# Optimization experiments

Measured on AMD Instinct MI355X. Metric: run time of the kernel, lower is better.

The kernel has to match this reference:

```python
import jax, jax.numpy as jnp
import numpy as np

N_NODES = 100000
N_EDGES = 800000
D_IN = 128
HOPS = 2
BN_EPS = 1e-5


def setup_inputs() -> dict:
    key = jax.random.key(0)
    ks = jax.random.split(key, 12)
    d_cat = D_IN * (HOPS + 1)  # 384
    inp = {
        "x": jax.random.normal(ks[0], (N_NODES, D_IN), dtype=jnp.float32),
        "edge_index": jax.random.randint(ks[1], (2, N_EDGES), 0, N_NODES, dtype=jnp.int32),
        "W0": jax.random.normal(ks[2], (HOPS + 1, D_IN, D_IN), dtype=jnp.float32) / np.sqrt(D_IN),
        "b0": jax.random.normal(ks[3], (HOPS + 1, D_IN), dtype=jnp.float32) * 0.01,
        "W1": jax.random.normal(ks[4], (HOPS + 1, d_cat, D_IN), dtype=jnp.float32) / np.sqrt(d_cat),
        "b1": jax.random.normal(ks[5], (HOPS + 1, D_IN), dtype=jnp.float32) * 0.01,
        "W2": jax.random.normal(ks[6], (HOPS + 1, d_cat, D_IN), dtype=jnp.float32) / np.sqrt(d_cat),
        "b2": jax.random.normal(ks[7], (HOPS + 1, D_IN), dtype=jnp.float32) * 0.01,
        "bn_gamma": jnp.ones((2, d_cat), dtype=jnp.float32),
        "bn_beta": jnp.zeros((2, d_cat), dtype=jnp.float32),
    }
    return inp


def _gcn_norm(edge_index, n):
    # gcn_norm(add_self_loops=False): deg over col, w_e = d^-1/2[row]*d^-1/2[col]
    row, col = edge_index[0], edge_index[1]
    deg = jax.ops.segment_sum(jnp.ones(row.shape[0], jnp.float32), col, num_segments=n)
    dinv = jnp.where(deg > 0, jax.lax.rsqrt(jnp.maximum(deg, 1.0)), 0.0)
    w = dinv[row] * dinv[col]
    return row, col, w


def _spmm(row, col, w, xj, n):
    # adj_t = SparseTensor(row=col, col=row, value=w): out[col_e] += w_e * x[row_e]
    return jax.ops.segment_sum(w[:, None] * xj[row], col, num_segments=n)


def _mixhop_layer(x, W, b, row, col, w, n):
    outs = [x @ W[0] + b[0]]
    for j in range(1, HOPS + 1):
        xj = x @ W[j] + b[j]
        for _ in range(j):
            xj = _spmm(row, col, w, xj, n)
        outs.append(xj)
    return jnp.concatenate(outs, axis=1)


def _bn(x, g, b):
    mu = jnp.mean(x, axis=0)
    var = jnp.mean(jnp.square(x - mu), axis=0)
    return (x - mu) * jax.lax.rsqrt(var + BN_EPS) * g + b


def reference(x, edge_index, W0, b0, W1, b1, W2, b2, bn_gamma, bn_beta):
    n = x.shape[0]
    row, col, w = _gcn_norm(edge_index, n)
    h = _mixhop_layer(x, W0, b0, row, col, w, n)
    h = jax.nn.relu(_bn(h, bn_gamma[0], bn_beta[0]))  # dropout: eval mode (identity)
    h = _mixhop_layer(h, W1, b1, row, col, w, n)
    h = jax.nn.relu(_bn(h, bn_gamma[1], bn_beta[1]))
    h = _mixhop_layer(h, W2, b2, row, col, w, n)
    return h
```

## Files before the change

kernel.cpp:

```cpp
#include <hip/hip_runtime.h>
#include <hip/hip_bf16.h>

#define NN 100000
#define NE 800000
#define DIN 128
#define DCAT 384
#define BN_EPS 1e-5

typedef __attribute__((ext_vector_type(8))) short bf16x8;
typedef __attribute__((ext_vector_type(4))) float f32x4;


__global__ void count_deg_k(const int* __restrict__ ei, int* __restrict__ deg) {
    int i = blockIdx.x * blockDim.x + threadIdx.x;
    if (i < NE) atomicAdd(&deg[ei[NE + i]], 1);
}

__global__ void dinv_k(const int* __restrict__ deg, float* __restrict__ dinv) {
    int i = blockIdx.x * blockDim.x + threadIdx.x;
    if (i < NN) {
        int d = deg[i];
        dinv[i] = (d > 0) ? rsqrtf((float)d) : 0.f;
    }
}

__global__ void scan1_k(const int* __restrict__ deg, int* __restrict__ out,
                        int* __restrict__ bsum) {
    __shared__ int s[1024];
    int i = blockIdx.x * 1024 + threadIdx.x;
    int v = (i < NN) ? deg[i] : 0;
    s[threadIdx.x] = v;
    __syncthreads();
    for (int off = 1; off < 1024; off <<= 1) {
        int t = (threadIdx.x >= off) ? s[threadIdx.x - off] : 0;
        __syncthreads();
        s[threadIdx.x] += t;
        __syncthreads();
    }
    if (i < NN) out[i] = s[threadIdx.x] - v;
    if (threadIdx.x == 1023) bsum[blockIdx.x] = s[1023];
}

__global__ void scan2_k(int* __restrict__ bsum, int nb) {
    if (threadIdx.x == 0) {
        int acc = 0;
        for (int b = 0; b < nb; ++b) { int v = bsum[b]; bsum[b] = acc; acc += v; }
    }
}

__global__ void scan3_k(int* __restrict__ ptr, int* __restrict__ cursor,
                        const int* __restrict__ bsum) {
    int i = blockIdx.x * 1024 + threadIdx.x;
    if (i < NN) {
        int p = ptr[i] + bsum[blockIdx.x];
        ptr[i] = p;
        cursor[i] = p;
    }
    if (i == NN) ptr[NN] = NE;
}

__global__ void scatter_k(const int* __restrict__ ei, const float* __restrict__ dinv,
                          int* __restrict__ cursor, int* __restrict__ crow,
                          float* __restrict__ cw) {
    int i = blockIdx.x * blockDim.x + threadIdx.x;
    if (i >= NE) return;
    int r = ei[i];
    int c = ei[NE + i];
    int p = atomicAdd(&cursor[c], 1);
    crow[p] = r;
    cw[p] = dinv[r] * dinv[c];
}


__device__ inline void split_trunc(float x, short& hi, short& lo) {
    unsigned u = __builtin_bit_cast(unsigned, x);
    hi = (short)(u >> 16);
    float hf = __builtin_bit_cast(float, u & 0xFFFF0000u);
    __hip_bfloat16 l = __float2bfloat16(x - hf);
    lo = *reinterpret_cast<short*>(&l);
}

__global__ void wsplit_k(const float* __restrict__ W, int K,
                         short* __restrict__ Wth, short* __restrict__ Wtl) {
    int i = blockIdx.x * 256 + threadIdx.x;
    if (i >= 3 * K * 128) return;
    int c = i & 127;
    int k = (i >> 7) % K;
    int j = i / (K * 128);
    short h, l;
    split_trunc(W[i], h, l);
    size_t o = (size_t)j * 128 * 384 + (size_t)c * 384 + k;
    Wth[o] = h;
    Wtl[o] = l;
}

#define GPITCH 40

__global__ __launch_bounds__(256, 2) void gemm3m_k(
    const float* __restrict__ X, int K,
    const short* __restrict__ Wth, const short* __restrict__ Wtl,
    const float* __restrict__ bias,
    float* __restrict__ o0, float* __restrict__ o1, float* __restrict__ o2) {
    __shared__ short As_h[128 * GPITCH];
    __shared__ short As_l[128 * GPITCH];
    __shared__ short Bs_h[128 * GPITCH];
    __shared__ short Bs_l[128 * GPITCH];

    const int j    = blockIdx.x;
    const int m0   = blockIdx.y * 128;
    const int t    = threadIdx.x;
    const int lane = t & 63;
    const int wv   = t >> 6;
    const int wr   = (wv >> 1) * 64;
    const int wc   = (wv & 1) * 64;
    const int lr   = lane & 15;
    const int lk   = lane >> 4;

    const short* Wh = Wth + (size_t)j * 128 * 384;
    const short* Wl = Wtl + (size_t)j * 128 * 384;

    f32x4 acc[4][4];
#pragma unroll
    for (int a = 0; a < 4; ++a)
#pragma unroll
        for (int b = 0; b < 4; ++b) acc[a][b] = (f32x4){0.f, 0.f, 0.f, 0.f};

    for (int kb = 0; kb < K; kb += 32) {
#pragma unroll
        for (int i = 0; i < 4; ++i) {
            int lin = t + i * 256;
            int row = lin >> 3, kq = lin & 7;
            int gr = m0 + row;
            if (gr >= NN) gr = NN - 1;
            float4 a4 = *(const float4*)(X + (size_t)gr * K + kb + kq * 4);
            short h0, l0, h1, l1, h2, l2, h3, l3;
            split_trunc(a4.x, h0, l0);
            split_trunc(a4.y, h1, l1);
            split_trunc(a4.z, h2, l2);
            split_trunc(a4.w, h3, l3);
            *(short4*)&As_h[row * GPITCH + kq * 4] = make_short4(h0, h1, h2, h3);
            *(short4*)&As_l[row * GPITCH + kq * 4] = make_short4(l0, l1, l2, l3);
        }
#pragma unroll
        for (int i = 0; i < 4; ++i) {
            int lin = t + i * 256;
            int col = lin >> 3, kq = lin & 7;
            short4 bh = *(const short4*)(Wh + (size_t)col * 384 + kb + kq * 4);
            short4 bl = *(const short4*)(Wl + (size_t)col * 384 + kb + kq * 4);
            *(short4*)&Bs_h[col * GPITCH + kq * 4] = bh;
            *(short4*)&Bs_l[col * GPITCH + kq * 4] = bl;
        }
        __syncthreads();

        bf16x8 ah[4], al[4];
#pragma unroll
        for (int mr = 0; mr < 4; ++mr) {
            int r = wr + mr * 16 + lr;
            ah[mr] = *(const bf16x8*)&As_h[r * GPITCH + lk * 8];
            al[mr] = *(const bf16x8*)&As_l[r * GPITCH + lk * 8];
        }
#pragma unroll
        for (int nc = 0; nc < 4; ++nc) {
            int c = wc + nc * 16 + lr;
            bf16x8 bh = *(const bf16x8*)&Bs_h[c * GPITCH + lk * 8];
            bf16x8 bl = *(const bf16x8*)&Bs_l[c * GPITCH + lk * 8];
#pragma unroll
            for (int mr = 0; mr < 4; ++mr) {
                f32x4 a = acc[mr][nc];
                a = __builtin_amdgcn_mfma_f32_16x16x32_bf16(al[mr], bh, a, 0, 0, 0);
                a = __builtin_amdgcn_mfma_f32_16x16x32_bf16(ah[mr], bl, a, 0, 0, 0);
                a = __builtin_amdgcn_mfma_f32_16x16x32_bf16(ah[mr], bh, a, 0, 0, 0);
                acc[mr][nc] = a;
            }
        }
        __syncthreads();
    }

    float* dst;
    int pitch;
    if (j == 0)      { dst = o0; pitch = DCAT; }
    else if (j == 1) { dst = o1; pitch = 128; }
    else             { dst = o2; pitch = 128; }

#pragma unroll
    for (int nc = 0; nc < 4; ++nc) {
        int col = wc + nc * 16 + lr;
        float bv = bias[j * 128 + col];
#pragma unroll
        for (int mr = 0; mr < 4; ++mr) {
            f32x4 a = acc[mr][nc];
#pragma unroll
            for (int r = 0; r < 4; ++r) {
                int row = m0 + wr + mr * 16 + lk * 4 + r;
                if (row < NN) dst[(size_t)row * pitch + col] = a[r] + bv;
            }
        }
    }
}

__global__ __launch_bounds__(256) void spmm_k(
    const int* __restrict__ ptr, const int* __restrict__ rows,
    const float* __restrict__ wv, const float* __restrict__ xin, int pin,
    float* __restrict__ xout, int pout) {
    int wid  = (blockIdx.x * blockDim.x + threadIdx.x) >> 6;
    int lane = threadIdx.x & 63;
    if (wid >= NN) return;
    int e0 = ptr[wid], e1 = ptr[wid + 1];
    float2 acc = make_float2(0.f, 0.f);
    for (int e = e0; e < e1; ++e) {
        int r   = rows[e];
        float w = wv[e];
        float2 v = ((const float2*)(xin + (size_t)r * pin))[lane];
        acc.x += w * v.x;
        acc.y += w * v.y;
    }
    ((float2*)(xout + (size_t)wid * pout))[lane] = acc;
}

#define BN_ROWS 256
#define BN_NBLK ((NN + BN_ROWS - 1) / BN_ROWS)

__global__ void bn_stats1_k(const float* __restrict__ H, float* __restrict__ partial) {
    int c  = threadIdx.x;
    int r0 = blockIdx.x * BN_ROWS;
    int r1 = min(r0 + BN_ROWS, NN);
    float s = 0.f, s2 = 0.f;
    for (int r = r0; r < r1; ++r) {
        float v = H[(size_t)r * DCAT + c];
        s  += v;
        s2 += v * v;
    }
    partial[blockIdx.x * 768 + c]       = s;
    partial[blockIdx.x * 768 + 384 + c] = s2;
}

__global__ void bn_finalize_k(const float* __restrict__ partial,
                              const float* __restrict__ g, const float* __restrict__ b,
                              float2* __restrict__ coef) {
    int c = threadIdx.x;
    double s = 0.0, s2 = 0.0;
    for (int i = 0; i < BN_NBLK; ++i) {
        s  += (double)partial[i * 768 + c];
        s2 += (double)partial[i * 768 + 384 + c];
    }
    double mu  = s / (double)NN;
    double var = s2 / (double)NN - mu * mu;
    double inv = 1.0 / sqrt(var + (double)BN_EPS);
    float scale = (float)((double)g[c] * inv);
    float shift = (float)((double)b[c] - mu * (double)g[c] * inv);
    coef[c] = make_float2(scale, shift);
}

__global__ void bn_apply_k(float* __restrict__ H, const float2* __restrict__ coef) {
    unsigned i = blockIdx.x * blockDim.x + threadIdx.x;
    if (i >= (unsigned)NN * 96u) return;
    float4 v = ((float4*)H)[i];
    int c4 = (int)(i % 96u) * 4;
    float2 s0 = coef[c4 + 0];
    float2 s1 = coef[c4 + 1];
    float2 s2 = coef[c4 + 2];
    float2 s3 = coef[c4 + 3];
    v.x = fmaxf(v.x * s0.x + s0.y, 0.f);
    v.y = fmaxf(v.y * s1.x + s1.y, 0.f);
    v.z = fmaxf(v.z * s2.x + s2.y, 0.f);
    v.w = fmaxf(v.w * s3.x + s3.y, 0.f);
    ((float4*)H)[i] = v;
}


static void run_layer(const float* X, int K, const float* W, const float* bias,
                      float* Hout, float* tmpA, float* tmpB,
                      short* Wth, short* Wtl,
                      const int* ptr, const int* crow, const float* cw,
                      hipStream_t stream) {
    int nw = 3 * K * 128;
    wsplit_k<<<(nw + 255) / 256, 256, 0, stream>>>(W, K, Wth, Wtl);
    dim3 g(3, (NN + 127) / 128);
    gemm3m_k<<<g, 256, 0, stream>>>(X, K, Wth, Wtl, bias, Hout, tmpA, tmpB);
    int sg = (NN * 64 + 255) / 256;
    spmm_k<<<sg, 256, 0, stream>>>(ptr, crow, cw, tmpA, 128, Hout + 128, DCAT);
    spmm_k<<<sg, 256, 0, stream>>>(ptr, crow, cw, tmpB, 128, tmpA, 128);
    spmm_k<<<sg, 256, 0, stream>>>(ptr, crow, cw, tmpA, 128, Hout + 256, DCAT);
}

static void run_bn(float* H, const float* g, const float* b,
                   float* partial, float2* coef, hipStream_t stream) {
    bn_stats1_k<<<BN_NBLK, 384, 0, stream>>>(H, partial);
    bn_finalize_k<<<1, 384, 0, stream>>>(partial, g, b, coef);
    unsigned n4 = (unsigned)NN * 96u;
    bn_apply_k<<<(n4 + 255) / 256, 256, 0, stream>>>(H, coef);
}

extern "C" void kernel_launch(void* const* d_in, const int* in_sizes, int n_in,
                              void* d_out, int out_size, void* d_ws, size_t ws_size,
                              hipStream_t stream) {
    const float* x        = (const float*)d_in[0];
    const int*   ei       = (const int*)d_in[1];
    const float* W0       = (const float*)d_in[2];
    const float* b0       = (const float*)d_in[3];
    const float* W1       = (const float*)d_in[4];
    const float* b1       = (const float*)d_in[5];
    const float* W2       = (const float*)d_in[6];
    const float* b2       = (const float*)d_in[7];
    const float* bn_gamma = (const float*)d_in[8];
    const float* bn_beta  = (const float*)d_in[9];
    float* out = (float*)d_out;

    char* p = (char*)d_ws;
    auto alloc = [&](size_t bytes) -> void* {
        void* r = (void*)p;
        p += (bytes + 511) & ~(size_t)511;
        return r;
    };
    float* Hws     = (float*)alloc((size_t)NN * DCAT * 4);
    float* tmpA    = (float*)alloc((size_t)NN * 128 * 4);
    float* tmpB    = (float*)alloc((size_t)NN * 128 * 4);
    int*   deg     = (int*)alloc((size_t)NN * 4);
    float* dinv    = (float*)alloc((size_t)NN * 4);
    int*   ptr     = (int*)alloc((size_t)(NN + 1) * 4);
    int*   cursor  = (int*)alloc((size_t)NN * 4);
    int*   bsum    = (int*)alloc(1024);
    int*   crow    = (int*)alloc((size_t)NE * 4);
    float* cw      = (float*)alloc((size_t)NE * 4);
    float* partial = (float*)alloc((size_t)BN_NBLK * 768 * 4);
    float2* coef   = (float2*)alloc(384 * 8);
    short* Wth     = (short*)alloc((size_t)3 * 128 * 384 * 2);
    short* Wtl     = (short*)alloc((size_t)3 * 128 * 384 * 2);

    hipMemsetAsync(deg, 0, (size_t)NN * 4, stream);
    count_deg_k<<<(NE + 255) / 256, 256, 0, stream>>>(ei, deg);
    dinv_k<<<(NN + 255) / 256, 256, 0, stream>>>(deg, dinv);
    int nsb = (NN + 1023) / 1024;
    scan1_k<<<nsb, 1024, 0, stream>>>(deg, ptr, bsum);
    scan2_k<<<1, 64, 0, stream>>>(bsum, nsb);
    scan3_k<<<nsb, 1024, 0, stream>>>(ptr, cursor, bsum);
    scatter_k<<<(NE + 255) / 256, 256, 0, stream>>>(ei, dinv, cursor, crow, cw);

    run_layer(x, DIN, W0, b0, out, tmpA, tmpB, Wth, Wtl, ptr, crow, cw, stream);
    run_bn(out, bn_gamma, bn_beta, partial, coef, stream);

    run_layer(out, DCAT, W1, b1, Hws, tmpA, tmpB, Wth, Wtl, ptr, crow, cw, stream);
    run_bn(Hws, bn_gamma + DCAT, bn_beta + DCAT, partial, coef, stream);

    run_layer(Hws, DCAT, W2, b2, out, tmpA, tmpB, Wth, Wtl, ptr, crow, cw, stream);
}
```

Before: 1.918 ms.

## Fuse BN apply into GEMM prologue, merge SpMMs, swizzle GEMM grid, unroll SpMM

Drops the separate batchnorm+ReLU pass by applying scale/shift/ReLU while loading GEMM A tiles, which removes a full read-write of the 100000x384 activation per layer. The first-hop SpMM and the first half of the two-hop SpMM are merged into one kernel that reads each edge list once and gathers both inputs. The GEMM grid is flattened with an XCD-aware swizzle so blocks sharing weights land on the same XCD. The SpMM edge loops are also unrolled for more memory-level parallelism. Risks: the GEMM A-load path gets heavier, and buffers are reused across layers (out/Hws as scratch), which needs careful aliasing.

New measurement: 1.702 ms. 1.13x faster.

```diff
diff --git a/kernel.cpp b/kernel.cpp
--- a/kernel.cpp
+++ b/kernel.cpp
@@ -100,14 +100,22 @@
     const float* __restrict__ X, int K,
     const short* __restrict__ Wth, const short* __restrict__ Wtl,
     const float* __restrict__ bias,
+    const float2* __restrict__ coef, int use_bn,
     float* __restrict__ o0, float* __restrict__ o1, float* __restrict__ o2) {
     __shared__ short As_h[128 * GPITCH];
     __shared__ short As_l[128 * GPITCH];
     __shared__ short Bs_h[128 * GPITCH];
     __shared__ short Bs_l[128 * GPITCH];
 
-    const int j    = blockIdx.x;
-    const int m0   = blockIdx.y * 128;
+    const int nwg = gridDim.x;
+    const int id  = blockIdx.x;
+    const int q = nwg >> 3, r = nwg & 7;
+    const int xcd = id & 7, ii = id >> 3;
+    const int swz = (xcd < r ? xcd * (q + 1) : r * (q + 1) + (xcd - r) * q) + ii;
+    const int j  = swz % 3;
+    const int my = swz / 3;
+    const int m0 = my * 128;
+
     const int t    = threadIdx.x;
     const int lane = t & 63;
     const int wv   = t >> 6;
@@ -133,6 +141,14 @@
             int gr = m0 + row;
             if (gr >= NN) gr = NN - 1;
             float4 a4 = *(const float4*)(X + (size_t)gr * K + kb + kq * 4);
+            if (use_bn) {
+                int c = kb + kq * 4;
+                float2 c0 = coef[c + 0], c1 = coef[c + 1], c2 = coef[c + 2], c3 = coef[c + 3];
+                a4.x = fmaxf(a4.x * c0.x + c0.y, 0.f);
+                a4.y = fmaxf(a4.y * c1.x + c1.y, 0.f);
+                a4.z = fmaxf(a4.z * c2.x + c2.y, 0.f);
+                a4.w = fmaxf(a4.w * c3.x + c3.y, 0.f);
+            }
             short h0, l0, h1, l1, h2, l2, h3, l3;
             split_trunc(a4.x, h0, l0);
             split_trunc(a4.y, h1, l1);
@@ -155,9 +171,9 @@
         bf16x8 ah[4], al[4];
 #pragma unroll
         for (int mr = 0; mr < 4; ++mr) {
-            int r = wr + mr * 16 + lr;
-            ah[mr] = *(const bf16x8*)&As_h[r * GPITCH + lk * 8];
-            al[mr] = *(const bf16x8*)&As_l[r * GPITCH + lk * 8];
+            int rr = wr + mr * 16 + lr;
+            ah[mr] = *(const bf16x8*)&As_h[rr * GPITCH + lk * 8];
+            al[mr] = *(const bf16x8*)&As_l[rr * GPITCH + lk * 8];
         }
 #pragma unroll
         for (int nc = 0; nc < 4; ++nc) {
@@ -190,12 +206,48 @@
         for (int mr = 0; mr < 4; ++mr) {
             f32x4 a = acc[mr][nc];
 #pragma unroll
-            for (int r = 0; r < 4; ++r) {
-                int row = m0 + wr + mr * 16 + lk * 4 + r;
-                if (row < NN) dst[(size_t)row * pitch + col] = a[r] + bv;
+            for (int rr = 0; rr < 4; ++rr) {
+                int row = m0 + wr + mr * 16 + lk * 4 + rr;
+                if (row < NN) dst[(size_t)row * pitch + col] = a[rr] + bv;
             }
         }
     }
+}
+
+__global__ __launch_bounds__(256) void spmm2_k(
+    const int* __restrict__ ptr, const int* __restrict__ rows,
+    const float* __restrict__ wv,
+    const float* __restrict__ inA, const float* __restrict__ inB,
+    float* __restrict__ outA, int poutA,
+    float* __restrict__ outB) {
+    int wid  = (blockIdx.x * blockDim.x + threadIdx.x) >> 6;
+    int lane = threadIdx.x & 63;
+    if (wid >= NN) return;
+    int e0 = ptr[wid], e1 = ptr[wid + 1];
+    float2 aA = make_float2(0.f, 0.f), aB = make_float2(0.f, 0.f);
+    int e = e0;
+    for (; e + 2 <= e1; e += 2) {
+        int   r0 = rows[e],  r1 = rows[e + 1];
+        float w0 = wv[e],    w1 = wv[e + 1];
+        float2 vA0 = ((const float2*)(inA + (size_t)r0 * 128))[lane];
+        float2 vB0 = ((const float2*)(inB + (size_t)r0 * 128))[lane];
+        float2 vA1 = ((const float2*)(inA + (size_t)r1 * 128))[lane];
+        float2 vB1 = ((const float2*)(inB + (size_t)r1 * 128))[lane];
+        aA.x += w0 * vA0.x; aA.y += w0 * vA0.y;
+        aB.x += w0 * vB0.x; aB.y += w0 * vB0.y;
+        aA.x += w1 * vA1.x; aA.y += w1 * vA1.y;
+        aB.x += w1 * vB1.x; aB.y += w1 * vB1.y;
+    }
+    if (e < e1) {
+        int   r0 = rows[e];
+        float w0 = wv[e];
+        float2 vA0 = ((const float2*)(inA + (size_t)r0 * 128))[lane];
+        float2 vB0 = ((const float2*)(inB + (size_t)r0 * 128))[lane];
+        aA.x += w0 * vA0.x; aA.y += w0 * vA0.y;
+        aB.x += w0 * vB0.x; aB.y += w0 * vB0.y;
+    }
+    ((float2*)(outA + (size_t)wid * poutA))[lane] = aA;
+    ((float2*)(outB + (size_t)wid * 128))[lane] = aB;
 }
 
 __global__ __launch_bounds__(256) void spmm_k(
@@ -207,12 +259,24 @@
     if (wid >= NN) return;
     int e0 = ptr[wid], e1 = ptr[wid + 1];
     float2 acc = make_float2(0.f, 0.f);
-    for (int e = e0; e < e1; ++e) {
-        int r   = rows[e];
-        float w = wv[e];
-        float2 v = ((const float2*)(xin + (size_t)r * pin))[lane];
-        acc.x += w * v.x;
-        acc.y += w * v.y;
+    int e = e0;
+    for (; e + 4 <= e1; e += 4) {
+        int   r0 = rows[e],     r1 = rows[e + 1], r2 = rows[e + 2], r3 = rows[e + 3];
+        float w0 = wv[e],       w1 = wv[e + 1],   w2 = wv[e + 2],   w3 = wv[e + 3];
+        float2 v0 = ((const float2*)(xin + (size_t)r0 * pin))[lane];
+        float2 v1 = ((const float2*)(xin + (size_t)r1 * pin))[lane];
+        float2 v2 = ((const float2*)(xin + (size_t)r2 * pin))[lane];
+        float2 v3 = ((const float2*)(xin + (size_t)r3 * pin))[lane];
+        acc.x += w0 * v0.x; acc.y += w0 * v0.y;
+        acc.x += w1 * v1.x; acc.y += w1 * v1.y;
+        acc.x += w2 * v2.x; acc.y += w2 * v2.y;
+        acc.x += w3 * v3.x; acc.y += w3 * v3.y;
+    }
+    for (; e < e1; ++e) {
+        int   r0 = rows[e];
+        float w0 = wv[e];
+        float2 v0 = ((const float2*)(xin + (size_t)r0 * pin))[lane];
+        acc.x += w0 * v0.x; acc.y += w0 * v0.y;
     }
     ((float2*)(xout + (size_t)wid * pout))[lane] = acc;
 }
@@ -251,44 +315,27 @@
     coef[c] = make_float2(scale, shift);
 }
 
-__global__ void bn_apply_k(float* __restrict__ H, const float2* __restrict__ coef) {
-    unsigned i = blockIdx.x * blockDim.x + threadIdx.x;
-    if (i >= (unsigned)NN * 96u) return;
-    float4 v = ((float4*)H)[i];
-    int c4 = (int)(i % 96u) * 4;
-    float2 s0 = coef[c4 + 0];
-    float2 s1 = coef[c4 + 1];
-    float2 s2 = coef[c4 + 2];
-    float2 s3 = coef[c4 + 3];
-    v.x = fmaxf(v.x * s0.x + s0.y, 0.f);
-    v.y = fmaxf(v.y * s1.x + s1.y, 0.f);
-    v.z = fmaxf(v.z * s2.x + s2.y, 0.f);
-    v.w = fmaxf(v.w * s3.x + s3.y, 0.f);
-    ((float4*)H)[i] = v;
-}
-
 
 static void run_layer(const float* X, int K, const float* W, const float* bias,
-                      float* Hout, float* tmpA, float* tmpB,
+                      const float2* coefIn, int use_bn,
+                      float* Hout, float* tmpA, float* tmpB, float* tmpC,
                       short* Wth, short* Wtl,
                       const int* ptr, const int* crow, const float* cw,
                       hipStream_t stream) {
     int nw = 3 * K * 128;
     wsplit_k<<<(nw + 255) / 256, 256, 0, stream>>>(W, K, Wth, Wtl);
-    dim3 g(3, (NN + 127) / 128);
-    gemm3m_k<<<g, 256, 0, stream>>>(X, K, Wth, Wtl, bias, Hout, tmpA, tmpB);
+    int nwg = 3 * ((NN + 127) / 128);
+    gemm3m_k<<<nwg, 256, 0, stream>>>(X, K, Wth, Wtl, bias, coefIn, use_bn,
+                                      Hout, tmpA, tmpB);
     int sg = (NN * 64 + 255) / 256;
-    spmm_k<<<sg, 256, 0, stream>>>(ptr, crow, cw, tmpA, 128, Hout + 128, DCAT);
-    spmm_k<<<sg, 256, 0, stream>>>(ptr, crow, cw, tmpB, 128, tmpA, 128);
-    spmm_k<<<sg, 256, 0, stream>>>(ptr, crow, cw, tmpA, 128, Hout + 256, DCAT);
-}
-
-static void run_bn(float* H, const float* g, const float* b,
-                   float* partial, float2* coef, hipStream_t stream) {
+    spmm2_k<<<sg, 256, 0, stream>>>(ptr, crow, cw, tmpA, tmpB, Hout + 128, DCAT, tmpC);
+    spmm_k<<<sg, 256, 0, stream>>>(ptr, crow, cw, tmpC, 128, Hout + 256, DCAT);
+}
+
+static void run_bn_stats(const float* H, const float* g, const float* b,
+                         float* partial, float2* coef, hipStream_t stream) {
     bn_stats1_k<<<BN_NBLK, 384, 0, stream>>>(H, partial);
     bn_finalize_k<<<1, 384, 0, stream>>>(partial, g, b, coef);
-    unsigned n4 = (unsigned)NN * 96u;
-    bn_apply_k<<<(n4 + 255) / 256, 256, 0, stream>>>(H, coef);
 }
 
 extern "C" void kernel_launch(void* const* d_in, const int* in_sizes, int n_in,
@@ -336,11 +383,14 @@
     scan3_k<<<nsb, 1024, 0, stream>>>(ptr, cursor, bsum);
     scatter_k<<<(NE + 255) / 256, 256, 0, stream>>>(ei, dinv, cursor, crow, cw);
 
-    run_layer(x, DIN, W0, b0, out, tmpA, tmpB, Wth, Wtl, ptr, crow, cw, stream);
-    run_bn(out, bn_gamma, bn_beta, partial, coef, stream);
-
-    run_layer(out, DCAT, W1, b1, Hws, tmpA, tmpB, Wth, Wtl, ptr, crow, cw, stream);
-    run_bn(Hws, bn_gamma + DCAT, bn_beta + DCAT, partial, coef, stream);
-
-    run_layer(Hws, DCAT, W2, b2, out, tmpA, tmpB, Wth, Wtl, ptr, crow, cw, stream);
-}
+    run_layer(x, DIN, W0, b0, coef, 0, out, tmpA, tmpB, Hws,
+              Wth, Wtl, ptr, crow, cw, stream);
+    run_bn_stats(out, bn_gamma, bn_beta, partial, coef, stream);
+
+    run_layer(out, DCAT, W1, b1, coef, 1, Hws, tmpA, tmpB, out,
+              Wth, Wtl, ptr, crow, cw, stream);
+    run_bn_stats(Hws, bn_gamma + DCAT, bn_beta + DCAT, partial, coef, stream);
+
+    run_layer(Hws, DCAT, W2, b2, coef, 1, out, tmpA, tmpB, Hws,
+              Wth, Wtl, ptr, crow, cw, stream);
+}
```
